# Kernel tuning notes

Measured on AMD Instinct MI355X. Metric: run time of the kernel, lower is better.

## Reference

```python
import jax, jax.numpy as jnp
import numpy as np
from jax import lax

B, CH, OUT = 2, 128, 128
H, W = 64, 64
S = 2            # scale_factor
K = 5            # up_kernel
COMP = 64        # compressed_channels
EK = 3           # encoder_kernel
K2 = K * K


def setup_inputs() -> dict:
    key = jax.random.key(0)
    ks = jax.random.split(key, 4)
    x = jax.random.normal(ks[0], (B, CH, H, W), jnp.float32)
    w_comp = jax.random.normal(ks[1], (COMP, CH), jnp.float32) * 0.05
    b_comp = jnp.zeros((COMP,), jnp.float32)
    # content encoder init std=0.001 (per normal_init in the source)
    w_enc = jax.random.normal(ks[2], (K2 * S * S, COMP, EK, EK), jnp.float32) * 0.001
    b_enc = jnp.zeros((K2 * S * S,), jnp.float32)
    w_proj = jax.random.normal(ks[3], (OUT, CH), jnp.float32) * 0.05
    b_proj = jnp.zeros((OUT,), jnp.float32)
    return {"x": x, "w_comp": w_comp, "b_comp": b_comp,
            "w_enc": w_enc, "b_enc": b_enc,
            "w_proj": w_proj, "b_proj": b_proj}


def _conv1x1(x, w, b):
    # x: (B,C,H,W), w: (O,C) -> (B,O,H,W)
    return jnp.einsum('bchw,oc->bohw', x, w) + b[None, :, None, None]


def reference(x, w_comp, b_comp, w_enc, b_enc, w_proj, b_proj):
    n, c, h, w = x.shape
    # 1) channel compressor (1x1 conv)
    compressed = _conv1x1(x, w_comp, b_comp)
    # 2) content encoder (3x3 conv, padding 1)
    kernel = lax.conv_general_dilated(
        compressed, w_enc, window_strides=(1, 1), padding=[(1, 1), (1, 1)],
        dimension_numbers=('NCHW', 'OIHW', 'NCHW')) + b_enc[None, :, None, None]
    # 3) kernel normalizer: pixel_shuffle(S) then softmax over k^2 positions
    # (B, K2*S*S, h, w) -> (B, K2, h*S, w*S)
    kernel = kernel.reshape(n, K2, S, S, h, w)
    kernel = kernel.transpose(0, 1, 4, 2, 5, 3).reshape(n, K2, h * S, w * S)
    kernel = jax.nn.softmax(kernel, axis=1)
    # 4) feature reassembly
    Hs, Ws = h * S, w * S
    x_up = jnp.repeat(jnp.repeat(x, S, axis=2), S, axis=3)   # nearest upsample
    p = (K // 2) * S                                         # unfold padding
    xp = jnp.pad(x_up, ((0, 0), (0, 0), (p, p), (p, p)))
    # unfold with kernel K, dilation S -> (B, C, K2, Hs, Ws), (kh, kw) row-major
    patches = jnp.stack(
        [xp[:, :, i * S:i * S + Hs, j * S:j * S + Ws]
         for i in range(K) for j in range(K)], axis=2)
    out = jnp.einsum('bkhw,bckhw->bchw', kernel, patches)
    # 5) projection (1x1 conv)
    return _conv1x1(out, w_proj, b_proj)
```

## Files before the change

### kernel.cpp

```cpp
#include <hip/hip_runtime.h>

constexpr int QQ = 100;

using short8 = __attribute__((ext_vector_type(8))) short;
using f32x4  = __attribute__((ext_vector_type(4))) float;

__device__ inline unsigned short f2bf(float f) {
    unsigned u = __float_as_uint(f);
    return (unsigned short)((u + 0x7FFF + ((u >> 16) & 1)) >> 16);
}
__device__ inline float bf2f(unsigned short us) {
    return __uint_as_float(((unsigned)us) << 16);
}

__global__ __launch_bounds__(256)
void k_prep(const float* __restrict__ x, const float* __restrict__ we,
            const float* __restrict__ wc, const float* __restrict__ be,
            const float* __restrict__ bc, const float* __restrict__ wproj,
            unsigned short* __restrict__ xt, unsigned short* __restrict__ weffR,
            float* __restrict__ beff, unsigned short* __restrict__ wpbR) {
    __shared__ float smf[2880];
    int blk = blockIdx.x, tid = threadIdx.x;
    if (blk < 512) {
        unsigned short* t = (unsigned short*)smf;
        int b = blk >> 8, y = (blk >> 2) & 63, cq = blk & 3;
        int lx = tid & 63, cg = tid >> 6;
        const float* xb = x + (b * 128 + cq * 32 + cg * 8) * 4096 + y * 64 + lx;
#pragma unroll
        for (int i = 0; i < 8; ++i)
            t[lx * 40 + cg * 8 + i] = f2bf(xb[i * 4096]);
        __syncthreads();
        int px = tid >> 2, j = tid & 3;
        *(short8*)(xt + (b * 4096 + y * 64 + px) * 128 + cq * 32 + j * 8)
            = *(const short8*)(t + px * 40 + j * 8);
        return;
    }
    if (blk < 624) {
        int q = blk - 512;
        float* we_s = smf;
        float* red  = smf + 576;
        if (q < QQ) {
            for (int idx = tid; idx < 576; idx += 256) we_s[idx] = we[q * 576 + idx];
            __syncthreads();
            int c = tid & 127, mh = tid >> 7;
            float acc[9];
#pragma unroll
            for (int k = 0; k < 9; ++k) acc[k] = 0.f;
            for (int m = 0; m < 32; ++m) {
                int mm = mh * 32 + m;
                float wv = wc[mm * 128 + c];
#pragma unroll
                for (int k = 0; k < 9; ++k) acc[k] += we_s[mm * 9 + k] * wv;
            }
#pragma unroll
            for (int k = 0; k < 9; ++k) red[(mh * 9 + k) * 128 + c] = acc[k];
            __syncthreads();
        }
        int mf = q >> 4, l15 = q & 15;
        for (int idx = tid; idx < 1152; idx += 256) {
            int kap = idx >> 7, r = idx & 127;
            float v = (q < QQ) ? (red[kap * 128 + r] + red[(9 + kap) * 128 + r]) : 0.f;
            int c32 = r >> 5, kgrp = (r >> 3) & 3, j = r & 7;
            weffR[(((kap * 4 + c32) * 7 + mf) * 64 + kgrp * 16 + l15) * 8 + j] = f2bf(v);
        }
        return;
    }
    if (tid < 128) {
        float s = 0.f;
        if (tid < QQ) {
            s = be[tid];
            for (int m = 0; m < 64; ++m) {
                float t2 = 0.f;
#pragma unroll
                for (int k = 0; k < 9; ++k) t2 += we[(tid * 64 + m) * 9 + k];
                s += t2 * bc[m];
            }
        }
        beff[tid] = s;
    }
    for (int idx = tid; idx < 16384; idx += 256) {
        int o = idx >> 7, c = idx & 127;
        int cs = c >> 5, kgrp = (c >> 3) & 3, j = c & 7;
        int mf = o >> 4, l15 = o & 15;
        wpbR[((cs * 8 + mf) * 64 + kgrp * 16 + l15) * 8 + j] = f2bf(wproj[idx]);
    }
}

__global__ __launch_bounds__(256)
void k_main(const unsigned short* __restrict__ xt, const unsigned short* __restrict__ weffR,
            const float* __restrict__ beff, const unsigned short* __restrict__ wpbR,
            const float* __restrict__ bproj, float* __restrict__ out) {
    __shared__ __align__(16) char smem[56448];
    unsigned short* xs = (unsigned short*)smem;
    float* sm          = (float*)(smem + 19584);
    float* psum        = (float*)(smem + 25984);
    unsigned short* re = (unsigned short*)(smem + 25984);

    int bid = blockIdx.x;
    int b = bid >> 8, rem = bid & 255;
    int ty = rem >> 3, tx = rem & 7;
    int tid = threadIdx.x;
    int lane = tid & 63, w = tid >> 6;
    int l15 = lane & 15, kgrp = lane >> 4;

    int R0 = ty * 2 - 2, C0 = tx * 8 - 2;
    for (int idx = tid; idx < 576; idx += 256) {
        int hp = idx >> 3, cq = idx & 7;
        int hy = hp / 12, hx = hp - hy * 12;
        int gr = R0 + hy, gc = C0 + hx;
        short8 v0 = {0,0,0,0,0,0,0,0}, v1 = {0,0,0,0,0,0,0,0};
        if ((unsigned)gr < 64u && (unsigned)gc < 64u) {
            const unsigned short* src = xt + (b * 4096 + gr * 64 + gc) * 128 + cq * 16;
            v0 = *(const short8*)src;
            v1 = *(const short8*)(src + 8);
        }
        *(short8*)&xs[hp * 136 + cq * 16]     = v0;
        *(short8*)&xs[hp * 136 + cq * 16 + 8] = v1;
    }
    __syncthreads();

    int ly = l15 >> 3, lx = l15 & 7;
    f32x4 acc[7];
#pragma unroll
    for (int mf = 0; mf < 7; ++mf) acc[mf] = f32x4{0.f, 0.f, 0.f, 0.f};
#pragma unroll
    for (int kap = 0; kap < 9; ++kap) {
        int dy = kap / 3, dx = kap % 3;
        short8 bfrag = *(const short8*)&xs[((ly + dy + 1) * 12 + lx + dx + 1) * 136
                                           + w * 32 + kgrp * 8];
        const unsigned short* wrk = weffR + ((kap * 4 + w) * 7) * 512 + lane * 8;
#pragma unroll
        for (int mf = 0; mf < 7; ++mf) {
            short8 af = *(const short8*)(wrk + mf * 512);
            acc[mf] = __builtin_amdgcn_mfma_f32_16x16x32_bf16(af, bfrag, acc[mf], 0, 0, 0);
        }
    }
#pragma unroll
    for (int mf = 0; mf < 7; ++mf)
#pragma unroll
        for (int r = 0; r < 4; ++r) {
            int q = mf * 16 + kgrp * 4 + r;
            psum[(w * 112 + q) * 17 + l15] = acc[mf][r];
        }
    __syncthreads();

    for (int idx = tid; idx < 1600; idx += 256) {
        int q = idx >> 4, lowpx = idx & 15;
        float v = psum[q * 17 + lowpx] + psum[(112 + q) * 17 + lowpx]
                + psum[(224 + q) * 17 + lowpx] + psum[(336 + q) * 17 + lowpx] + beff[q];
        sm[(q >> 2) * 64 + lowpx * 4 + (q & 3)] = v;
    }
    __syncthreads();

    {
        int e = tid >> 2, kg = tid & 3;
        float v[7];
        float m = -1e30f;
#pragma unroll
        for (int j = 0; j < 7; ++j) {
            int k = kg + 4 * j;
            float val = (k < 25) ? sm[k * 64 + e] : -1e30f;
            v[j] = val; m = fmaxf(m, val);
        }
        m = fmaxf(m, __shfl_xor(m, 1));
        m = fmaxf(m, __shfl_xor(m, 2));
        float s = 0.f;
#pragma unroll
        for (int j = 0; j < 7; ++j) {
            int k = kg + 4 * j;
            if (k < 25) { v[j] = __expf(v[j] - m); s += v[j]; }
        }
        s += __shfl_xor(s, 1);
        s += __shfl_xor(s, 2);
        float inv = 1.f / s;
#pragma unroll
        for (int j = 0; j < 7; ++j) {
            int k = kg + 4 * j;
            if (k < 25) sm[k * 64 + e] = v[j] * inv;
        }
    }
    __syncthreads();

    {
        int lowpx = tid & 15, cgrp = tid >> 4;
        int ly2 = lowpx >> 3, lx2 = lowpx & 7;
        float racc[8][4];
#pragma unroll
        for (int cc = 0; cc < 8; ++cc)
#pragma unroll
            for (int s = 0; s < 4; ++s) racc[cc][s] = 0.f;
#pragma unroll
        for (int k = 0; k < 25; ++k) {
            int i = k / 5, j = k % 5;
            float4 wk4 = *(const float4*)&sm[k * 64 + lowpx * 4];
            short8 tap8 = *(const short8*)&xs[((ly2 + i) * 12 + (lx2 + j)) * 136 + cgrp * 8];
#pragma unroll
            for (int cc = 0; cc < 8; ++cc) {
                float tap = bf2f((unsigned short)tap8[cc]);
                racc[cc][0] += wk4.x * tap;
                racc[cc][1] += wk4.y * tap;
                racc[cc][2] += wk4.z * tap;
                racc[cc][3] += wk4.w * tap;
            }
        }
#pragma unroll
        for (int s = 0; s < 4; ++s) {
            int p = (ly2 * 2 + (s >> 1)) * 16 + lx2 * 2 + (s & 1);
            short8 pk;
#pragma unroll
            for (int cc = 0; cc < 8; ++cc) pk[cc] = (short)f2bf(racc[cc][s]);
            *(short8*)&re[p * 136 + cgrp * 8] = pk;
        }
    }
    __syncthreads();

    f32x4 pacc[8];
#pragma unroll
    for (int mf = 0; mf < 8; ++mf) pacc[mf] = f32x4{0.f, 0.f, 0.f, 0.f};
#pragma unroll
    for (int cs = 0; cs < 4; ++cs) {
        short8 bfrag = *(const short8*)&re[(w * 16 + l15) * 136 + cs * 32 + kgrp * 8];
        const unsigned short* wrp = wpbR + (cs * 8) * 512 + lane * 8;
#pragma unroll
        for (int mf = 0; mf < 8; ++mf) {
            short8 af = *(const short8*)(wrp + mf * 512);
            pacc[mf] = __builtin_amdgcn_mfma_f32_16x16x32_bf16(af, bfrag, pacc[mf], 0, 0, 0);
        }
    }
    int hs = ty * 4 + w, ws = tx * 16 + l15;
    float* ob = out + (b * 128) * 16384 + hs * 128 + ws;
#pragma unroll
    for (int mf = 0; mf < 8; ++mf)
#pragma unroll
        for (int r = 0; r < 4; ++r) {
            int o = mf * 16 + kgrp * 4 + r;
            ob[o * 16384] = pacc[mf][r] + bproj[o];
        }
}

extern "C" void kernel_launch(void* const* d_in, const int* in_sizes, int n_in,
                              void* d_out, int out_size, void* d_ws, size_t ws_size,
                              hipStream_t stream) {
    const float* x      = (const float*)d_in[0];
    const float* w_comp = (const float*)d_in[1];
    const float* b_comp = (const float*)d_in[2];
    const float* w_enc  = (const float*)d_in[3];
    const float* b_enc  = (const float*)d_in[4];
    const float* w_proj = (const float*)d_in[5];
    const float* b_proj = (const float*)d_in[6];
    float* out = (float*)d_out;

    char* base = (char*)d_ws;
    unsigned short* xt    = (unsigned short*)(base);
    unsigned short* weffR = (unsigned short*)(base + 2097152);
    float*          beff  = (float*)         (base + 2355200);
    unsigned short* wpbR  = (unsigned short*)(base + 2355712);

    k_prep<<<625, 256, 0, stream>>>(x, w_enc, w_comp, b_enc, b_comp, w_proj,
                                    xt, weffR, beff, wpbR);
    k_main<<<512, 256, 0, stream>>>(xt, weffR, beff, wpbR, b_proj, out);
}
```

Baseline: 106.8 us.

## Split encoder MFMA work across waves by output fragment instead of channel slice

Each wave previously handled a 32-channel slice for all 7 output fragments, which required a shared-memory partial-sum buffer, a block barrier and a 4-way reduction. Now each wave owns 1-2 output fragments and loops over all four channel slices itself, so accumulators are complete in registers and are written with bias directly into the softmax buffer. This removes the psum buffer, one barrier and the reduction pass, and cuts LDS use, which may raise occupancy. The cost is uneven work across waves (wave 3 does half as much) and more weight-fragment loads per wave.

```diff
diff --git a/kernel.cpp b/kernel.cpp
--- a/kernel.cpp
+++ b/kernel.cpp
@@ -90,10 +90,9 @@
 void k_main(const unsigned short* __restrict__ xt, const unsigned short* __restrict__ weffR,
             const float* __restrict__ beff, const unsigned short* __restrict__ wpbR,
             const float* __restrict__ bproj, float* __restrict__ out) {
-    __shared__ __align__(16) char smem[56448];
+    __shared__ __align__(16) char smem[43392];
     unsigned short* xs = (unsigned short*)smem;
     float* sm          = (float*)(smem + 19584);
-    float* psum        = (float*)(smem + 25984);
     unsigned short* re = (unsigned short*)(smem + 25984);
 
     int bid = blockIdx.x;
@@ -102,6 +101,17 @@
     int tid = threadIdx.x;
     int lane = tid & 63, w = tid >> 6;
     int l15 = lane & 15, kgrp = lane >> 4;
+    int fb = w * 2;
+    int nf = (w < 3) ? 2 : 1;
+
+    float bq[2][4];
+#pragma unroll
+    for (int j = 0; j < 2; ++j)
+#pragma unroll
+        for (int r = 0; r < 4; ++r) {
+            int q = (fb + j) * 16 + kgrp * 4 + r;
+            bq[j][r] = beff[q];
+        }
 
     int R0 = ty * 2 - 2, C0 = tx * 8 - 2;
     for (int idx = tid; idx < 576; idx += 256) {
@@ -120,35 +130,35 @@
     __syncthreads();
 
     int ly = l15 >> 3, lx = l15 & 7;
-    f32x4 acc[7];
-#pragma unroll
-    for (int mf = 0; mf < 7; ++mf) acc[mf] = f32x4{0.f, 0.f, 0.f, 0.f};
+    f32x4 acc[2];
+    acc[0] = f32x4{0.f, 0.f, 0.f, 0.f};
+    acc[1] = f32x4{0.f, 0.f, 0.f, 0.f};
 #pragma unroll
     for (int kap = 0; kap < 9; ++kap) {
         int dy = kap / 3, dx = kap % 3;
-        short8 bfrag = *(const short8*)&xs[((ly + dy + 1) * 12 + lx + dx + 1) * 136
-                                           + w * 32 + kgrp * 8];
-        const unsigned short* wrk = weffR + ((kap * 4 + w) * 7) * 512 + lane * 8;
-#pragma unroll
-        for (int mf = 0; mf < 7; ++mf) {
-            short8 af = *(const short8*)(wrk + mf * 512);
-            acc[mf] = __builtin_amdgcn_mfma_f32_16x16x32_bf16(af, bfrag, acc[mf], 0, 0, 0);
-        }
-    }
-#pragma unroll
-    for (int mf = 0; mf < 7; ++mf)
-#pragma unroll
-        for (int r = 0; r < 4; ++r) {
-            int q = mf * 16 + kgrp * 4 + r;
-            psum[(w * 112 + q) * 17 + l15] = acc[mf][r];
-        }
-    __syncthreads();
-
-    for (int idx = tid; idx < 1600; idx += 256) {
-        int q = idx >> 4, lowpx = idx & 15;
-        float v = psum[q * 17 + lowpx] + psum[(112 + q) * 17 + lowpx]
-                + psum[(224 + q) * 17 + lowpx] + psum[(336 + q) * 17 + lowpx] + beff[q];
-        sm[(q >> 2) * 64 + lowpx * 4 + (q & 3)] = v;
+        const unsigned short* xrow = &xs[((ly + dy + 1) * 12 + lx + dx + 1) * 136];
+#pragma unroll
+        for (int cs = 0; cs < 4; ++cs) {
+            short8 bfrag = *(const short8*)&xrow[cs * 32 + kgrp * 8];
+            const unsigned short* wrk = weffR + ((kap * 4 + cs) * 7 + fb) * 512 + lane * 8;
+            acc[0] = __builtin_amdgcn_mfma_f32_16x16x32_bf16(
+                *(const short8*)wrk, bfrag, acc[0], 0, 0, 0);
+            if (w < 3)
+                acc[1] = __builtin_amdgcn_mfma_f32_16x16x32_bf16(
+                    *(const short8*)(wrk + 512), bfrag, acc[1], 0, 0, 0);
+        }
+    }
+#pragma unroll
+    for (int j = 0; j < 2; ++j) {
+        if (j < nf) {
+            int f = fb + j;
+#pragma unroll
+            for (int r = 0; r < 4; ++r) {
+                int q = f * 16 + kgrp * 4 + r;
+                if (q < QQ)
+                    sm[(q >> 2) * 64 + l15 * 4 + (q & 3)] = acc[j][r] + bq[j][r];
+            }
+        }
     }
     __syncthreads();
 
```

Measured after the change: 118.5 us. 11.0% more time.

## Double k_main block to 512 threads and redistribute work across eight waves

Applied to the files above, without the earlier changes.

Raises k_main to 512 threads (8 waves) per block. The encoder MFMA stage is split by channel-pair and output-fragment group, with only two partial sums to reduce. The softmax uses 8 lanes per element, and reassembly handles 4 channels per thread. The projection GEMM is re-split so each wave owns 16 output channels across 4 pixel rows, which also shrinks shared memory. The aim is more latency hiding and shorter per-thread serial chains on a grid of only 512 blocks. The cost is wave-imbalanced MFMA work, since one encoder group has a single fragment, and more barrier participants.

```diff
diff --git a/kernel.cpp b/kernel.cpp
--- a/kernel.cpp
+++ b/kernel.cpp
@@ -2,8 +2,9 @@
 
 constexpr int QQ = 100;
 
-using short8 = __attribute__((ext_vector_type(8))) short;
-using f32x4  = __attribute__((ext_vector_type(4))) float;
+using short8  = __attribute__((ext_vector_type(8))) short;
+using short4v = __attribute__((ext_vector_type(4))) short;
+using f32x4   = __attribute__((ext_vector_type(4))) float;
 
 __device__ inline unsigned short f2bf(float f) {
     unsigned u = __float_as_uint(f);
@@ -86,11 +87,11 @@
     }
 }
 
-__global__ __launch_bounds__(256)
+__global__ __launch_bounds__(512)
 void k_main(const unsigned short* __restrict__ xt, const unsigned short* __restrict__ weffR,
             const float* __restrict__ beff, const unsigned short* __restrict__ wpbR,
             const float* __restrict__ bproj, float* __restrict__ out) {
-    __shared__ __align__(16) char smem[56448];
+    __shared__ __align__(16) char smem[43392];
     unsigned short* xs = (unsigned short*)smem;
     float* sm          = (float*)(smem + 19584);
     float* psum        = (float*)(smem + 25984);
@@ -104,7 +105,7 @@
     int l15 = lane & 15, kgrp = lane >> 4;
 
     int R0 = ty * 2 - 2, C0 = tx * 8 - 2;
-    for (int idx = tid; idx < 576; idx += 256) {
+    for (int idx = tid; idx < 576; idx += 512) {
         int hp = idx >> 3, cq = idx & 7;
         int hy = hp / 12, hx = hp - hy * 12;
         int gr = R0 + hy, gc = C0 + hx;
@@ -119,63 +120,68 @@
     }
     __syncthreads();
 
+    int kp = w & 1, mg = w >> 1;
+    int mf0 = mg * 2;
+    bool two = (mg < 3);
     int ly = l15 >> 3, lx = l15 & 7;
-    f32x4 acc[7];
-#pragma unroll
-    for (int mf = 0; mf < 7; ++mf) acc[mf] = f32x4{0.f, 0.f, 0.f, 0.f};
+    f32x4 acc0 = {0.f, 0.f, 0.f, 0.f}, acc1 = {0.f, 0.f, 0.f, 0.f};
 #pragma unroll
     for (int kap = 0; kap < 9; ++kap) {
         int dy = kap / 3, dx = kap % 3;
-        short8 bfrag = *(const short8*)&xs[((ly + dy + 1) * 12 + lx + dx + 1) * 136
-                                           + w * 32 + kgrp * 8];
-        const unsigned short* wrk = weffR + ((kap * 4 + w) * 7) * 512 + lane * 8;
-#pragma unroll
-        for (int mf = 0; mf < 7; ++mf) {
-            short8 af = *(const short8*)(wrk + mf * 512);
-            acc[mf] = __builtin_amdgcn_mfma_f32_16x16x32_bf16(af, bfrag, acc[mf], 0, 0, 0);
-        }
-    }
-#pragma unroll
-    for (int mf = 0; mf < 7; ++mf)
-#pragma unroll
-        for (int r = 0; r < 4; ++r) {
-            int q = mf * 16 + kgrp * 4 + r;
-            psum[(w * 112 + q) * 17 + l15] = acc[mf][r];
-        }
-    __syncthreads();
-
-    for (int idx = tid; idx < 1600; idx += 256) {
+        const unsigned short* xrow = &xs[((ly + dy + 1) * 12 + lx + dx + 1) * 136];
+#pragma unroll
+        for (int cc = 0; cc < 2; ++cc) {
+            int cs = kp * 2 + cc;
+            short8 bfrag = *(const short8*)&xrow[cs * 32 + kgrp * 8];
+            const unsigned short* wrk = weffR + ((kap * 4 + cs) * 7 + mf0) * 512 + lane * 8;
+            acc0 = __builtin_amdgcn_mfma_f32_16x16x32_bf16(
+                *(const short8*)wrk, bfrag, acc0, 0, 0, 0);
+            if (two)
+                acc1 = __builtin_amdgcn_mfma_f32_16x16x32_bf16(
+                    *(const short8*)(wrk + 512), bfrag, acc1, 0, 0, 0);
+        }
+    }
+#pragma unroll
+    for (int r = 0; r < 4; ++r) {
+        int q0 = mf0 * 16 + kgrp * 4 + r;
+        psum[(kp * 112 + q0) * 17 + l15] = acc0[r];
+        if (two) psum[(kp * 112 + q0 + 16) * 17 + l15] = acc1[r];
+    }
+    __syncthreads();
+
+    for (int idx = tid; idx < 1600; idx += 512) {
         int q = idx >> 4, lowpx = idx & 15;
-        float v = psum[q * 17 + lowpx] + psum[(112 + q) * 17 + lowpx]
-                + psum[(224 + q) * 17 + lowpx] + psum[(336 + q) * 17 + lowpx] + beff[q];
+        float v = psum[q * 17 + lowpx] + psum[(112 + q) * 17 + lowpx] + beff[q];
         sm[(q >> 2) * 64 + lowpx * 4 + (q & 3)] = v;
     }
     __syncthreads();
 
     {
-        int e = tid >> 2, kg = tid & 3;
-        float v[7];
+        int e = tid >> 3, kg = tid & 7;
+        float v[4];
         float m = -1e30f;
 #pragma unroll
-        for (int j = 0; j < 7; ++j) {
-            int k = kg + 4 * j;
+        for (int j = 0; j < 4; ++j) {
+            int k = kg + 8 * j;
             float val = (k < 25) ? sm[k * 64 + e] : -1e30f;
             v[j] = val; m = fmaxf(m, val);
         }
         m = fmaxf(m, __shfl_xor(m, 1));
         m = fmaxf(m, __shfl_xor(m, 2));
+        m = fmaxf(m, __shfl_xor(m, 4));
         float s = 0.f;
 #pragma unroll
-        for (int j = 0; j < 7; ++j) {
-            int k = kg + 4 * j;
+        for (int j = 0; j < 4; ++j) {
+            int k = kg + 8 * j;
             if (k < 25) { v[j] = __expf(v[j] - m); s += v[j]; }
         }
         s += __shfl_xor(s, 1);
         s += __shfl_xor(s, 2);
+        s += __shfl_xor(s, 4);
         float inv = 1.f / s;
 #pragma unroll
-        for (int j = 0; j < 7; ++j) {
-            int k = kg + 4 * j;
+        for (int j = 0; j < 4; ++j) {
+            int k = kg + 8 * j;
             if (k < 25) sm[k * 64 + e] = v[j] * inv;
         }
     }
@@ -184,19 +190,19 @@
     {
         int lowpx = tid & 15, cgrp = tid >> 4;
         int ly2 = lowpx >> 3, lx2 = lowpx & 7;
-        float racc[8][4];
-#pragma unroll
-        for (int cc = 0; cc < 8; ++cc)
+        float racc[4][4];
+#pragma unroll
+        for (int cc = 0; cc < 4; ++cc)
 #pragma unroll
             for (int s = 0; s < 4; ++s) racc[cc][s] = 0.f;
 #pragma unroll
         for (int k = 0; k < 25; ++k) {
             int i = k / 5, j = k % 5;
             float4 wk4 = *(const float4*)&sm[k * 64 + lowpx * 4];
-            short8 tap8 = *(const short8*)&xs[((ly2 + i) * 12 + (lx2 + j)) * 136 + cgrp * 8];
-#pragma unroll
-            for (int cc = 0; cc < 8; ++cc) {
-                float tap = bf2f((unsigned short)tap8[cc]);
+            short4v tap4 = *(const short4v*)&xs[((ly2 + i) * 12 + (lx2 + j)) * 136 + cgrp * 4];
+#pragma unroll
+            for (int cc = 0; cc < 4; ++cc) {
+                float tap = bf2f((unsigned short)tap4[cc]);
                 racc[cc][0] += wk4.x * tap;
                 racc[cc][1] += wk4.y * tap;
                 racc[cc][2] += wk4.z * tap;
@@ -206,36 +212,37 @@
 #pragma unroll
         for (int s = 0; s < 4; ++s) {
             int p = (ly2 * 2 + (s >> 1)) * 16 + lx2 * 2 + (s & 1);
-            short8 pk;
-#pragma unroll
-            for (int cc = 0; cc < 8; ++cc) pk[cc] = (short)f2bf(racc[cc][s]);
-            *(short8*)&re[p * 136 + cgrp * 8] = pk;
-        }
-    }
-    __syncthreads();
-
-    f32x4 pacc[8];
-#pragma unroll
-    for (int mf = 0; mf < 8; ++mf) pacc[mf] = f32x4{0.f, 0.f, 0.f, 0.f};
+            short4v pk;
+#pragma unroll
+            for (int cc = 0; cc < 4; ++cc) pk[cc] = (short)f2bf(racc[cc][s]);
+            *(short4v*)&re[p * 136 + cgrp * 4] = pk;
+        }
+    }
+    __syncthreads();
+
+    f32x4 pacc[4];
+#pragma unroll
+    for (int nf = 0; nf < 4; ++nf) pacc[nf] = f32x4{0.f, 0.f, 0.f, 0.f};
 #pragma unroll
     for (int cs = 0; cs < 4; ++cs) {
-        short8 bfrag = *(const short8*)&re[(w * 16 + l15) * 136 + cs * 32 + kgrp * 8];
-        const unsigned short* wrp = wpbR + (cs * 8) * 512 + lane * 8;
-#pragma unroll
-        for (int mf = 0; mf < 8; ++mf) {
-            short8 af = *(const short8*)(wrp + mf * 512);
-            pacc[mf] = __builtin_amdgcn_mfma_f32_16x16x32_bf16(af, bfrag, pacc[mf], 0, 0, 0);
-        }
-    }
-    int hs = ty * 4 + w, ws = tx * 16 + l15;
-    float* ob = out + (b * 128) * 16384 + hs * 128 + ws;
-#pragma unroll
-    for (int mf = 0; mf < 8; ++mf)
-#pragma unroll
-        for (int r = 0; r < 4; ++r) {
-            int o = mf * 16 + kgrp * 4 + r;
-            ob[o * 16384] = pacc[mf][r] + bproj[o];
-        }
+        short8 af = *(const short8*)(wpbR + (cs * 8 + w) * 512 + lane * 8);
+#pragma unroll
+        for (int nf = 0; nf < 4; ++nf) {
+            short8 bfrag = *(const short8*)&re[(nf * 16 + l15) * 136 + cs * 32 + kgrp * 8];
+            pacc[nf] = __builtin_amdgcn_mfma_f32_16x16x32_bf16(af, bfrag, pacc[nf], 0, 0, 0);
+        }
+    }
+    float bo[4];
+#pragma unroll
+    for (int r = 0; r < 4; ++r) bo[r] = bproj[w * 16 + kgrp * 4 + r];
+#pragma unroll
+    for (int nf = 0; nf < 4; ++nf) {
+        int hs = ty * 4 + nf;
+        float* ob = out + (b * 128 + w * 16 + kgrp * 4) * 16384 + hs * 128 + tx * 16 + l15;
+#pragma unroll
+        for (int r = 0; r < 4; ++r)
+            ob[r * 16384] = pacc[nf][r] + bo[r];
+    }
 }
 
 extern "C" void kernel_launch(void* const* d_in, const int* in_sizes, int n_in,
@@ -258,5 +265,5 @@
 
     k_prep<<<625, 256, 0, stream>>>(x, w_enc, w_comp, b_enc, b_comp, w_proj,
                                     xt, weffR, beff, wpbR);
-    k_main<<<512, 256, 0, stream>>>(xt, weffR, beff, wpbR, b_proj, out);
-}
+    k_main<<<512, 512, 0, stream>>>(xt, weffR, beff, wpbR, b_proj, out);
+}
```

New measurement: 107.5 us. No clear change (+0.7%).
